# Optimization experiments

Hardware: AMD Instinct MI355X
Metric: run time of the kernel (lower is better)

## Reference

```python
import jax, jax.numpy as jnp
import numpy as np

OUT_F, IN_F = 16384, 4096
TOKENS = 8192
PALETTE = 256


def setup_inputs() -> dict:
    key = jax.random.key(0)
    k1, k2, k3, k4 = jax.random.split(key, 4)
    input = jax.random.normal(k1, (TOKENS, IN_F), dtype=jnp.float32)
    weight_idx = jax.random.randint(k2, (OUT_F, IN_F), 0, PALETTE, dtype=jnp.int32)
    lookup_table = jax.random.normal(k3, (PALETTE,), dtype=jnp.float32)
    bias = jax.random.normal(k4, (OUT_F,), dtype=jnp.float32)
    return {"input": input, "weight_idx": weight_idx, "lookup_table": lookup_table, "bias": bias}


def reference(input, weight_idx, lookup_table, bias):
    # Dequantize: LUT gather expands uint8 indices to full-precision weights [out, in]
    full_weights = lookup_table[weight_idx]
    # F.linear: y = x @ W^T + b
    return jnp.einsum('ti,oi->to', input, full_weights) + bias
```

## Files before the change

kernel.cpp:

```cpp
#include <hip/hip_runtime.h>
#include <stdint.h>

#define TOKENS 8192
#define OUT_F  16384
#define IN_F   4096

typedef short bf16x8 __attribute__((ext_vector_type(8)));
typedef float f32x4  __attribute__((ext_vector_type(4)));

__device__ __forceinline__ unsigned short bf16_rne(float f) {
    union { float f; unsigned int u; } v; v.f = f;
    unsigned int u = v.u;
    u += 0x7fffu + ((u >> 16) & 1u);
    return (unsigned short)(u >> 16);
}

__device__ __forceinline__ unsigned int pack_bf16x2(float a, float b) {
    return (unsigned int)bf16_rne(a) | ((unsigned int)bf16_rne(b) << 16);
}

__device__ __forceinline__ void async_cp16(const void* gptr, void* ldsptr) {
    __builtin_amdgcn_global_load_lds(
        (const __attribute__((address_space(1))) unsigned int*)gptr,
        (__attribute__((address_space(3))) unsigned int*)ldsptr,
        16, 0, 0);
}

__global__ __launch_bounds__(256) void cvt_input_kernel(
    const float* __restrict__ in, unsigned short* __restrict__ out, int n8)
{
    int i = blockIdx.x * 256 + threadIdx.x;
    if (i >= n8) return;
    size_t base = (size_t)i * 8;
    float4 a = *(const float4*)(in + base);
    float4 b = *(const float4*)(in + base + 4);
    uint4 p;
    p.x = pack_bf16x2(a.x, a.y);  p.y = pack_bf16x2(a.z, a.w);
    p.z = pack_bf16x2(b.x, b.y);  p.w = pack_bf16x2(b.z, b.w);
    *(uint4*)(out + base) = p;
}

__global__ __launch_bounds__(256) void dequant_kernel(
    const int* __restrict__ idx, const float* __restrict__ lut,
    unsigned short* __restrict__ out, int n8)
{
    __shared__ float slut[256];
    slut[threadIdx.x] = lut[threadIdx.x];
    __syncthreads();
    int i = blockIdx.x * 256 + threadIdx.x;
    if (i >= n8) return;
    size_t base = (size_t)i * 8;
    int4 i0 = *(const int4*)(idx + base);
    int4 i1 = *(const int4*)(idx + base + 4);
    uint4 p;
    p.x = pack_bf16x2(slut[i0.x], slut[i0.y]);
    p.y = pack_bf16x2(slut[i0.z], slut[i0.w]);
    p.z = pack_bf16x2(slut[i1.x], slut[i1.y]);
    p.w = pack_bf16x2(slut[i1.z], slut[i1.w]);
    *(uint4*)(out + base) = p;
}

__global__ __launch_bounds__(512, 2) void palett_gemm256(
    const unsigned short* __restrict__ A,
    const unsigned short* __restrict__ B,
    const float* __restrict__ bias,
    float* __restrict__ out)
{
    __shared__ __align__(16) char sm[131072];

    const int t    = threadIdx.x;
    const int w    = t >> 6;
    const int l    = t & 63;
    const int quad = l >> 4;
    const int r16  = l & 15;
    const int wr   = w >> 2;
    const int wc   = w & 3;

    const int orig = blockIdx.y * gridDim.x + blockIdx.x;
    const int swzb = (orig & 7) * 256 + (orig >> 3);
    const int n0   = (swzb & 63) << 8;
    const int m0   = (swzb >> 6) << 8;

    const int srow = w * 16 + (l >> 3);
    const int scol = ((l & 7) ^ (l >> 3)) << 3;
    const unsigned short* pA = A + (size_t)(m0 + srow) * IN_F + scol;
    const unsigned short* pB = B + (size_t)(n0 + srow) * IN_F + scol;

    const int cswz  = (r16 & 7) << 4;
    const int col0  = (quad * 16) ^ cswz;
    const int col1  = (64 + quad * 16) ^ cswz;
    const int arow  = r16 * 128;
    const int abase = wr * 16384;
    const int bbase = 32768 + (wc >> 1) * 16384 + (wc & 1) * 8192;

    f32x4  acc[8][4] = {};
    bf16x8 rA[4][2], rB0[2][2], rB1[2][2];

#define BARRIER() asm volatile("s_barrier" ::: "memory")

#define STAGE(P, HOFF, LOFF, KOFF) do {                                          \
    async_cp16((P) + (size_t)(HOFF) * IN_F + (KOFF), sm + (LOFF) + w * 2048);    \
    async_cp16((P) + (size_t)((HOFF) + 8) * IN_F + (KOFF),                       \
               sm + (LOFF) + w * 2048 + 1024);                                   \
} while (0)

#define READ_A(RB_, MH) do {                                                     \
    _Pragma("unroll")                                                            \
    for (int i_ = 0; i_ < 4; ++i_) {                                             \
        rA[i_][0] = *(const bf16x8*)(sm + (RB_) + abase + ((MH)*4 + i_)*2048 + arow + col0); \
        rA[i_][1] = *(const bf16x8*)(sm + (RB_) + abase + ((MH)*4 + i_)*2048 + arow + col1); \
    }                                                                            \
} while (0)

#define READ_B(DST, RB_, NH) do {                                                \
    _Pragma("unroll")                                                            \
    for (int j_ = 0; j_ < 2; ++j_) {                                             \
        DST[j_][0] = *(const bf16x8*)(sm + (RB_) + bbase + ((NH)*2 + j_)*2048 + arow + col0); \
        DST[j_][1] = *(const bf16x8*)(sm + (RB_) + bbase + ((NH)*2 + j_)*2048 + arow + col1); \
    }                                                                            \
} while (0)

#define MFMA_Q(MH, NH, RB) do {                                                  \
    _Pragma("unroll")                                                            \
    for (int i_ = 0; i_ < 4; ++i_) {                                             \
        _Pragma("unroll")                                                        \
        for (int j_ = 0; j_ < 2; ++j_) {                                         \
            acc[(MH)*4+i_][(NH)*2+j_] = __builtin_amdgcn_mfma_f32_16x16x32_bf16( \
                rA[i_][0], RB[j_][0], acc[(MH)*4+i_][(NH)*2+j_], 0, 0, 0);       \
            acc[(MH)*4+i_][(NH)*2+j_] = __builtin_amdgcn_mfma_f32_16x16x32_bf16( \
                rA[i_][1], RB[j_][1], acc[(MH)*4+i_][(NH)*2+j_], 0, 0, 0);       \
        }                                                                        \
    }                                                                            \
} while (0)

#define TILE(RB_, WB_, KOFF) do {                                                \
                                                \
    STAGE(pA, 0, (WB_) + 0, KOFF);                                               \
    asm volatile("s_waitcnt vmcnt(2)" ::: "memory");                             \
    BARRIER();                                                                   \
    READ_A(RB_, 0);                                                              \
    READ_B(rB0, RB_, 0);                                                         \
    __builtin_amdgcn_s_setprio(1);                                               \
    MFMA_Q(0, 0, rB0);                                                           \
    __builtin_amdgcn_s_setprio(0);                                               \
    READ_B(rB1, RB_, 1);                                                         \
    BARRIER();                                                                   \
                            \
    STAGE(pA, 128, (WB_) + 16384, KOFF);                                         \
    BARRIER();                                                                   \
    __builtin_amdgcn_s_setprio(1);                                               \
    MFMA_Q(0, 1, rB1);                                                           \
    __builtin_amdgcn_s_setprio(0);                                               \
    READ_A(RB_, 1);                                                              \
    BARRIER();                                                                   \
                                                                    \
    STAGE(pB, 0, (WB_) + 32768, KOFF);                                           \
    BARRIER();                                                                   \
    __builtin_amdgcn_s_setprio(1);                                               \
    MFMA_Q(1, 0, rB0);                                                           \
    __builtin_amdgcn_s_setprio(0);                                               \
    BARRIER();                                                                   \
                                                                    \
    STAGE(pB, 128, (WB_) + 49152, KOFF);                                         \
    BARRIER();                                                                   \
    __builtin_amdgcn_s_setprio(1);                                               \
    MFMA_Q(1, 1, rB1);                                                           \
    __builtin_amdgcn_s_setprio(0);                                               \
    BARRIER();                                                                   \
} while (0)

    STAGE(pA, 0,   0,     0);
    STAGE(pA, 128, 16384, 0);
    STAGE(pB, 0,   32768, 0);
    STAGE(pB, 128, 49152, 0);

#pragma unroll 1
    for (int it = 0; it < 32; ++it) {
        const int k1 = (2 * it + 1) * 64;
        const int k2 = ((2 * it + 2) & 63) * 64;
        TILE(0,     65536, k1);
        TILE(65536, 0,     k2);
    }
    asm volatile("s_waitcnt vmcnt(0)" ::: "memory");

#undef TILE
#undef MFMA_Q
#undef READ_B
#undef READ_A
#undef STAGE
#undef BARRIER

    float bj[4];
#pragma unroll
    for (int j = 0; j < 4; ++j) bj[j] = bias[n0 + wc * 64 + j * 16 + r16];

#pragma unroll
    for (int mf = 0; mf < 8; ++mf) {
        const int mrow = m0 + wr * 128 + mf * 16 + quad * 4;
#pragma unroll
        for (int nf = 0; nf < 4; ++nf) {
            const int n = n0 + wc * 64 + nf * 16 + r16;
#pragma unroll
            for (int v = 0; v < 4; ++v)
                out[(size_t)(mrow + v) * OUT_F + n] = acc[mf][nf][v] + bj[nf];
        }
    }
}

__global__ __launch_bounds__(256) void palett_gemm_fused(
    const float* __restrict__ Af,
    const int* __restrict__ Widx,
    const float* __restrict__ lut,
    const float* __restrict__ bias,
    float* __restrict__ out)
{
    __shared__ __align__(16) unsigned short smA[128 * 32];
    __shared__ __align__(16) unsigned short smB[128 * 32];
    __shared__ float slut[256];

    const int t    = threadIdx.x;
    const int w    = t >> 6;
    const int l    = t & 63;
    const int quad = l >> 4;
    const int r16  = l & 15;
    const int wr   = w >> 1;
    const int wc   = w & 1;

    const int m0 = blockIdx.y * 128;
    const int n0 = blockIdx.x * 128;

    const int g0  = t * 8;
    const int row = g0 >> 5;
    const int col = g0 & 31;

    char* const smA_c = (char*)smA;
    char* const smB_c = (char*)smB;

    slut[t] = lut[t];
    __syncthreads();

    uint32_t aoff[4], boff[4];
#pragma unroll
    for (int i = 0; i < 4; ++i) {
        aoff[i] = (uint32_t)(((wr * 64 + i * 16 + r16) * 32 + quad * 8) * 2);
        boff[i] = (uint32_t)(((wc * 64 + i * 16 + r16) * 32 + quad * 8) * 2);
    }

    f32x4 acc[4][4] = {};

    const float* af0 = Af + (size_t)(m0 + row) * IN_F + col;
    const float* af1 = Af + (size_t)(m0 + row + 64) * IN_F + col;
    const int*   wi0 = Widx + (size_t)(n0 + row) * IN_F + col;
    const int*   wi1 = Widx + (size_t)(n0 + row + 64) * IN_F + col;

    for (int k0 = 0; k0 < IN_F; k0 += 32) {
        float4 x0 = *(const float4*)(af0 + k0);
        float4 x1 = *(const float4*)(af0 + k0 + 4);
        uint4 p;
        p.x = pack_bf16x2(x0.x, x0.y); p.y = pack_bf16x2(x0.z, x0.w);
        p.z = pack_bf16x2(x1.x, x1.y); p.w = pack_bf16x2(x1.z, x1.w);
        *(uint4*)(smA_c + t * 16) = p;
        x0 = *(const float4*)(af1 + k0);
        x1 = *(const float4*)(af1 + k0 + 4);
        p.x = pack_bf16x2(x0.x, x0.y); p.y = pack_bf16x2(x0.z, x0.w);
        p.z = pack_bf16x2(x1.x, x1.y); p.w = pack_bf16x2(x1.z, x1.w);
        *(uint4*)(smA_c + 4096 + t * 16) = p;

        int4 j0 = *(const int4*)(wi0 + k0);
        int4 j1 = *(const int4*)(wi0 + k0 + 4);
        p.x = pack_bf16x2(slut[j0.x], slut[j0.y]);
        p.y = pack_bf16x2(slut[j0.z], slut[j0.w]);
        p.z = pack_bf16x2(slut[j1.x], slut[j1.y]);
        p.w = pack_bf16x2(slut[j1.z], slut[j1.w]);
        *(uint4*)(smB_c + t * 16) = p;
        j0 = *(const int4*)(wi1 + k0);
        j1 = *(const int4*)(wi1 + k0 + 4);
        p.x = pack_bf16x2(slut[j0.x], slut[j0.y]);
        p.y = pack_bf16x2(slut[j0.z], slut[j0.w]);
        p.z = pack_bf16x2(slut[j1.x], slut[j1.y]);
        p.w = pack_bf16x2(slut[j1.z], slut[j1.w]);
        *(uint4*)(smB_c + 4096 + t * 16) = p;
        __syncthreads();

        bf16x8 afr[4], bfr[4];
#pragma unroll
        for (int i = 0; i < 4; ++i) afr[i] = *(const bf16x8*)(smA_c + aoff[i]);
#pragma unroll
        for (int j = 0; j < 4; ++j) bfr[j] = *(const bf16x8*)(smB_c + boff[j]);
#pragma unroll
        for (int i = 0; i < 4; ++i)
#pragma unroll
            for (int j = 0; j < 4; ++j)
                acc[i][j] = __builtin_amdgcn_mfma_f32_16x16x32_bf16(
                    afr[i], bfr[j], acc[i][j], 0, 0, 0);
        __syncthreads();
    }

    float bj[4];
#pragma unroll
    for (int j = 0; j < 4; ++j) bj[j] = bias[n0 + wc * 64 + j * 16 + r16];

#pragma unroll
    for (int i = 0; i < 4; ++i) {
        const int mbase = m0 + wr * 64 + i * 16 + quad * 4;
#pragma unroll
        for (int j = 0; j < 4; ++j) {
            const int n = n0 + wc * 64 + j * 16 + r16;
#pragma unroll
            for (int v = 0; v < 4; ++v) {
                out[(size_t)(mbase + v) * OUT_F + n] = acc[i][j][v] + bj[j];
            }
        }
    }
}

extern "C" void kernel_launch(void* const* d_in, const int* in_sizes, int n_in,
                              void* d_out, int out_size, void* d_ws, size_t ws_size,
                              hipStream_t stream) {
    const float* input = (const float*)d_in[0];
    const int*   widx  = (const int*)d_in[1];
    const float* lut   = (const float*)d_in[2];
    const float* bias  = (const float*)d_in[3];
    float* out = (float*)d_out;

    const size_t aBytes = (size_t)TOKENS * IN_F * sizeof(unsigned short);
    const size_t bBytes = (size_t)OUT_F  * IN_F * sizeof(unsigned short);

    if (ws_size >= aBytes + bBytes) {
        unsigned short* wsA = (unsigned short*)d_ws;
        unsigned short* wsB = (unsigned short*)((char*)d_ws + aBytes);
        const int nA8 = (TOKENS * IN_F) / 8;
        const int nB8 = (OUT_F  * IN_F) / 8;
        cvt_input_kernel<<<(nA8 + 255) / 256, 256, 0, stream>>>(input, wsA, nA8);
        dequant_kernel<<<(nB8 + 255) / 256, 256, 0, stream>>>(widx, lut, wsB, nB8);
        dim3 grid2(OUT_F / 256, TOKENS / 256);
        palett_gemm256<<<grid2, 512, 0, stream>>>(wsA, wsB, bias, out);
    } else {
        dim3 grid(OUT_F / 128, TOKENS / 128);
        palett_gemm_fused<<<grid, 256, 0, stream>>>(input, widx, lut, bias, out);
    }
}
```

Baseline: 1.642 ms.

## Restructure GEMM main loop to prefetch A two tiles ahead and cut barriers

Reworks the double-buffered LDS pipeline so B for the next k-tile is staged at the start of each tile, and A is prefetched further ahead into the buffer just consumed, once an lgkmcnt wait confirms all LDS reads finished. The number of barriers per tile drops from eight to four, and the vmcnt wait moves to the end of the tile. The aim is more overlap between global-to-LDS loads and MFMA work with less synchronization stall. The trade-off is more complex buffer-reuse ordering, with a risk of races if the wait counts are wrong.

```diff
diff --git a/kernel.cpp b/kernel.cpp
--- a/kernel.cpp
+++ b/kernel.cpp
@@ -133,53 +133,57 @@
     }                                                                            \
 } while (0)
 
-#define TILE(RB_, WB_, KOFF) do {                                                \
-                                                \
-    STAGE(pA, 0, (WB_) + 0, KOFF);                                               \
-    asm volatile("s_waitcnt vmcnt(2)" ::: "memory");                             \
-    BARRIER();                                                                   \
+#define TILE(RB_, WB_, KB_, KA_) do {                                            \
+                                        \
+    STAGE(pB, 0,   (WB_) + 32768, KB_);                                          \
+    STAGE(pB, 128, (WB_) + 49152, KB_);                                          \
     READ_A(RB_, 0);                                                              \
     READ_B(rB0, RB_, 0);                                                         \
     __builtin_amdgcn_s_setprio(1);                                               \
     MFMA_Q(0, 0, rB0);                                                           \
     __builtin_amdgcn_s_setprio(0);                                               \
+    BARRIER();                                                                   \
+        \
     READ_B(rB1, RB_, 1);                                                         \
-    BARRIER();                                                                   \
-                            \
-    STAGE(pA, 128, (WB_) + 16384, KOFF);                                         \
-    BARRIER();                                                                   \
     __builtin_amdgcn_s_setprio(1);                                               \
     MFMA_Q(0, 1, rB1);                                                           \
     __builtin_amdgcn_s_setprio(0);                                               \
     READ_A(RB_, 1);                                                              \
-    BARRIER();                                                                   \
-                                                                    \
-    STAGE(pB, 0, (WB_) + 32768, KOFF);                                           \
-    BARRIER();                                                                   \
+    asm volatile("s_waitcnt lgkmcnt(0)" ::: "memory");                           \
+    BARRIER();           \
+                                             \
+    STAGE(pA, 0,   (RB_) + 0,     KA_);                                          \
+    STAGE(pA, 128, (RB_) + 16384, KA_);                                          \
     __builtin_amdgcn_s_setprio(1);                                               \
     MFMA_Q(1, 0, rB0);                                                           \
     __builtin_amdgcn_s_setprio(0);                                               \
     BARRIER();                                                                   \
-                                                                    \
-    STAGE(pB, 128, (WB_) + 49152, KOFF);                                         \
-    BARRIER();                                                                   \
+             \
     __builtin_amdgcn_s_setprio(1);                                               \
     MFMA_Q(1, 1, rB1);                                                           \
     __builtin_amdgcn_s_setprio(0);                                               \
+    asm volatile("s_waitcnt vmcnt(4)" ::: "memory");                             \
     BARRIER();                                                                   \
 } while (0)
 
-    STAGE(pA, 0,   0,     0);
-    STAGE(pA, 128, 16384, 0);
-    STAGE(pB, 0,   32768, 0);
-    STAGE(pB, 128, 49152, 0);
+    STAGE(pA, 0,   0,             0);
+    STAGE(pA, 128, 16384,         0);
+    STAGE(pB, 0,   32768,         0);
+    STAGE(pB, 128, 49152,         0);
+    STAGE(pA, 0,   65536 + 0,     64);
+    STAGE(pA, 128, 65536 + 16384, 64);
+    asm volatile("s_waitcnt vmcnt(4)" ::: "memory");
+    BARRIER();
 
 #pragma unroll 1
     for (int it = 0; it < 32; ++it) {
-        const int k1 = (2 * it + 1) * 64;
-        const int k2 = ((2 * it + 2) & 63) * 64;
-        TILE(0,     65536, k1);
-        TILE(65536, 0,     k2);
+        const int tt = 2 * it;
+        const int kB0 = ((tt + 1) & 63) * 64;
+        const int kA0 = ((tt + 2) & 63) * 64;
+        const int kB1 = ((tt + 2) & 63) * 64;
+        const int kA1 = ((tt + 3) & 63) * 64;
+        TILE(0,     65536, kB0, kA0);
+        TILE(65536, 0,     kB1, kA1);
     }
     asm volatile("s_waitcnt vmcnt(0)" ::: "memory");
 
```

New measurement: 1.580 ms. 1.04x faster.
